# Optimization experiments

Hardware: AMD Instinct MI355X
Metric: run time of the kernel (lower is better)

## Reference

```python
import jax, jax.numpy as jnp
import numpy as np

N, E, G = 50000, 800000, 512
IN, HID, H1, H2, OUT = 128, 32, 8, 4, 128
D1, D2 = HID * H1, HID * H2  # 256, 128


def _ln(x, g, b, eps=1e-5):
    m = x.mean(-1, keepdims=True)
    v = jnp.var(x, axis=-1, keepdims=True)
    return (x - m) * jax.lax.rsqrt(v + eps) * g + b


def _gat_conv(x, W, a_src, a_dst, bias, edge_index, heads, ch, concat):
    # PyG GATConv (eval): h = xW per head; e = leakyrelu(a_src.h_src + a_dst.h_dst);
    # segment softmax over destination nodes; scatter-sum messages; self-loops added.
    n = x.shape[0]
    h = (x @ W).reshape(n, heads, ch)                      # [N,H,C]
    asrc = jnp.sum(h * a_src, axis=-1)                     # [N,H]
    adst = jnp.sum(h * a_dst, axis=-1)                     # [N,H]
    loop = jnp.arange(n)
    src = jnp.concatenate([edge_index[0], loop])           # [E+N]
    dst = jnp.concatenate([edge_index[1], loop])
    e = jax.nn.leaky_relu(asrc[src] + adst[dst], 0.2)      # [E+N,H]
    emax = jax.ops.segment_max(e, dst, num_segments=n)
    p = jnp.exp(e - emax[dst])
    denom = jax.ops.segment_sum(p, dst, num_segments=n)
    alpha = p / (denom[dst] + 1e-16)                       # [E+N,H]
    out = jax.ops.segment_sum(h[src] * alpha[..., None], dst, num_segments=n)  # [N,H,C]
    out = out.reshape(n, heads * ch) if concat else out.mean(axis=1)
    return out + bias


def setup_inputs():
    key = jax.random.key(0)
    ks = jax.random.split(key, 32)
    g = lambda i, shape, s=0.05: jax.random.normal(ks[i], shape, dtype=jnp.float32) * s
    inp = {
        "x": jax.random.normal(ks[0], (N, IN), dtype=jnp.float32),
        "edge_index": jax.random.randint(ks[1], (2, E), 0, N, dtype=jnp.int32),
        "batch": jnp.sort(jax.random.randint(ks[2], (N,), 0, G, dtype=jnp.int32)),
        # GAT layer 1: in 128 -> 8 heads x 32
        "W1": g(3, (IN, H1 * HID)), "a_src1": g(4, (H1, HID)), "a_dst1": g(5, (H1, HID)),
        "b1": jnp.zeros((D1,), jnp.float32), "g1": jnp.ones((D1,), jnp.float32), "be1": jnp.zeros((D1,), jnp.float32),
        "pw1": g(6, (IN, D1)), "pb1": jnp.zeros((D1,), jnp.float32),
        # GAT layer 2: 256 -> 4 heads x 32
        "W2": g(7, (D1, H2 * HID)), "a_src2": g(8, (H2, HID)), "a_dst2": g(9, (H2, HID)),
        "b2": jnp.zeros((D2,), jnp.float32), "g2": jnp.ones((D2,), jnp.float32), "be2": jnp.zeros((D2,), jnp.float32),
        "pw2": g(10, (D1, D2)), "pb2": jnp.zeros((D2,), jnp.float32),
        # GAT layer 3: 128 -> 1 head x 128, concat=False
        "W3": g(11, (D2, OUT)), "a_src3": g(12, (1, OUT)), "a_dst3": g(13, (1, OUT)),
        "b3": jnp.zeros((OUT,), jnp.float32), "g3": jnp.ones((OUT,), jnp.float32), "be3": jnp.zeros((OUT,), jnp.float32),
        "pw3": g(14, (D2, OUT)), "pb3": jnp.zeros((OUT,), jnp.float32),
    }
    return inp


def reference(x, edge_index, batch,
              W1, a_src1, a_dst1, b1, g1, be1, pw1, pb1,
              W2, a_src2, a_dst2, b2, g2, be2, pw2, pb2,
              W3, a_src3, a_dst3, b3, g3, be3, pw3, pb3):
    h1 = _gat_conv(x, W1, a_src1, a_dst1, b1, edge_index, H1, HID, True)
    h1 = jax.nn.elu(_ln(h1, g1, be1) + (x @ pw1 + pb1))
    h2 = _gat_conv(h1, W2, a_src2, a_dst2, b2, edge_index, H2, HID, True)
    h2 = jax.nn.elu(_ln(h2, g2, be2) + (h1 @ pw2 + pb2))
    h3 = _gat_conv(h2, W3, a_src3, a_dst3, b3, edge_index, 1, OUT, False)
    h3 = jax.nn.elu(_ln(h3, g3, be3) + (h2 @ pw3 + pb3))
    # jk='last' -> h3; global mean pool per graph
    sums = jax.ops.segment_sum(h3, batch, num_segments=G)              # [G,OUT]
    cnt = jax.ops.segment_sum(jnp.ones((N,), h3.dtype), batch, num_segments=G)
    return sums / jnp.maximum(cnt, 1.0)[:, None]
```

## Files before the change

### kernel.cpp

```cpp
#include <hip/hip_runtime.h>
#include <hip/hip_fp16.h>
#include <math.h>


typedef _Float16 f16x8 __attribute__((ext_vector_type(8)));
typedef float f32x4 __attribute__((ext_vector_type(4)));

static __device__ __forceinline__ float h2f(unsigned short u) {
  return __half2float(__builtin_bit_cast(__half, u));
}
static __device__ __forceinline__ unsigned short f2h(float f) {
  return __builtin_bit_cast(unsigned short, __float2half_rn(f));
}
static __device__ __forceinline__ float hlo(unsigned int w) {
  return __low2float(__builtin_bit_cast(__half2, w));
}
static __device__ __forceinline__ float hhi(unsigned int w) {
  return __high2float(__builtin_bit_cast(__half2, w));
}
static __device__ __forceinline__ float wave_sum(float v) {
#pragma unroll
  for (int off = 1; off < 64; off <<= 1) v += __shfl_xor(v, off, 64);
  return v;
}

template <int K, int C, int H, bool ATOMIC>
__global__ __launch_bounds__(256) void fused_gemm_kernel(
    const unsigned short* __restrict__ A, const unsigned short* __restrict__ Bp1,
    const unsigned short* __restrict__ Bp2, const float* __restrict__ bias2,
    const float* __restrict__ a_src, const float* __restrict__ a_dst,
    unsigned short* __restrict__ C1, unsigned short* __restrict__ C2,
    float* __restrict__ asrc, float* __restrict__ adst, int Ncols) {
  const int lane = threadIdx.x & 63;
  const int w = threadIdx.x >> 6;
  const int ml = lane & 15, kq = lane >> 4;
  const int row0 = blockIdx.y * 64 + (w >> 1) * 32;
  const int colt0 = blockIdx.x * 4 + (w & 1) * 2;
  constexpr int KB = K / 32;

  f32x4 w00 = {}, w01 = {}, w10 = {}, w11 = {};
  f32x4 p00 = {}, p01 = {}, p10 = {}, p11 = {};
  const unsigned short* a0 = A + (size_t)(row0 + ml) * K + kq * 8;
  const unsigned short* b1 = Bp1 + ((size_t)colt0 * KB * 64 + lane) * 8;
  const unsigned short* b2 = Bp2 + ((size_t)colt0 * KB * 64 + lane) * 8;
#pragma unroll
  for (int kb = 0; kb < KB; kb++) {
    f16x8 af0 = __builtin_bit_cast(f16x8, *(const uint4*)(a0 + kb * 32));
    f16x8 af1 = __builtin_bit_cast(f16x8, *(const uint4*)(a0 + 16 * K + kb * 32));
    f16x8 bw0 = __builtin_bit_cast(f16x8, *(const uint4*)(b1 + (size_t)kb * 512));
    f16x8 bw1 = __builtin_bit_cast(f16x8, *(const uint4*)(b1 + (size_t)(KB + kb) * 512));
    f16x8 bp0 = __builtin_bit_cast(f16x8, *(const uint4*)(b2 + (size_t)kb * 512));
    f16x8 bp1 = __builtin_bit_cast(f16x8, *(const uint4*)(b2 + (size_t)(KB + kb) * 512));
    w00 = __builtin_amdgcn_mfma_f32_16x16x32_f16(af0, bw0, w00, 0, 0, 0);
    w01 = __builtin_amdgcn_mfma_f32_16x16x32_f16(af0, bw1, w01, 0, 0, 0);
    w10 = __builtin_amdgcn_mfma_f32_16x16x32_f16(af1, bw0, w10, 0, 0, 0);
    w11 = __builtin_amdgcn_mfma_f32_16x16x32_f16(af1, bw1, w11, 0, 0, 0);
    p00 = __builtin_amdgcn_mfma_f32_16x16x32_f16(af0, bp0, p00, 0, 0, 0);
    p01 = __builtin_amdgcn_mfma_f32_16x16x32_f16(af0, bp1, p01, 0, 0, 0);
    p10 = __builtin_amdgcn_mfma_f32_16x16x32_f16(af1, bp0, p10, 0, 0, 0);
    p11 = __builtin_amdgcn_mfma_f32_16x16x32_f16(af1, bp1, p11, 0, 0, 0);
  }
  const int c0 = colt0 * 16 + ml, c1 = c0 + 16;
  const float bi0 = bias2[c0], bi1 = bias2[c1];
#pragma unroll
  for (int r = 0; r < 4; r++) {
    const size_t rA = (size_t)(row0 + kq * 4 + r);
    const size_t rB = rA + 16;
    C1[rA * Ncols + c0] = f2h(w00[r]);
    C1[rA * Ncols + c1] = f2h(w01[r]);
    C1[rB * Ncols + c0] = f2h(w10[r]);
    C1[rB * Ncols + c1] = f2h(w11[r]);
    C2[rA * Ncols + c0] = f2h(p00[r] + bi0);
    C2[rA * Ncols + c1] = f2h(p01[r] + bi1);
    C2[rB * Ncols + c0] = f2h(p10[r] + bi0);
    C2[rB * Ncols + c1] = f2h(p11[r] + bi1);
  }

  const int hh = (colt0 * 16) / C;
  const float aS0 = a_src[hh * C + (c0 % C)], aS1 = a_src[hh * C + (c1 % C)];
  const float aD0 = a_dst[hh * C + (c0 % C)], aD1 = a_dst[hh * C + (c1 % C)];
  float pS0[4], pD0[4], pS1[4], pD1[4];
#pragma unroll
  for (int r = 0; r < 4; r++) {
    pS0[r] = w00[r] * aS0 + w01[r] * aS1;
    pD0[r] = w00[r] * aD0 + w01[r] * aD1;
    pS1[r] = w10[r] * aS0 + w11[r] * aS1;
    pD1[r] = w10[r] * aD0 + w11[r] * aD1;
  }
#pragma unroll
  for (int off = 1; off < 16; off <<= 1) {
#pragma unroll
    for (int r = 0; r < 4; r++) {
      pS0[r] += __shfl_xor(pS0[r], off);
      pD0[r] += __shfl_xor(pD0[r], off);
      pS1[r] += __shfl_xor(pS1[r], off);
      pD1[r] += __shfl_xor(pD1[r], off);
    }
  }
  if (ml < 4) {
    const int r = ml;
    const int rowA = row0 + kq * 4 + r;
    const int rowB = rowA + 16;
    if constexpr (ATOMIC) {
      atomicAdd(&asrc[rowA * H + hh], pS0[r]);
      atomicAdd(&adst[rowA * H + hh], pD0[r]);
      atomicAdd(&asrc[rowB * H + hh], pS1[r]);
      atomicAdd(&adst[rowB * H + hh], pD1[r]);
    } else {
      asrc[rowA * H + hh] = pS0[r];
      adst[rowA * H + hh] = pD0[r];
      asrc[rowB * H + hh] = pS1[r];
      adst[rowB * H + hh] = pD1[r];
    }
  }
}

static __device__ __forceinline__ void repack_one(const float* B, unsigned short* Bp,
                                                  int K, int Ncols, int idx) {
  const int KB = K >> 5;
  const int lane = idx & 63;
  const int kb = (idx >> 6) % KB;
  const int nt = idx / (KB << 6);
  const int ml = lane & 15, kq = lane >> 4;
  unsigned short* dst = Bp + (size_t)idx * 8;
#pragma unroll
  for (int j = 0; j < 8; j++)
    dst[j] = f2h(B[(size_t)(kb * 32 + kq * 8 + j) * Ncols + nt * 16 + ml]);
}

__global__ __launch_bounds__(256) void repack_all_kernel(
    const float* W1, const float* pw1, const float* W2, const float* pw2,
    const float* W3, const float* pw3, unsigned short* BpW1, unsigned short* BpP1,
    unsigned short* BpW2, unsigned short* BpP2, unsigned short* BpW3,
    unsigned short* BpP3) {
  int idx = blockIdx.x * 256 + threadIdx.x;
  if (idx < 4096) { repack_one(W1, BpW1, 128, 256, idx); return; }
  idx -= 4096;
  if (idx < 4096) { repack_one(pw1, BpP1, 128, 256, idx); return; }
  idx -= 4096;
  if (idx < 4096) { repack_one(W2, BpW2, 256, 128, idx); return; }
  idx -= 4096;
  if (idx < 4096) { repack_one(pw2, BpP2, 256, 128, idx); return; }
  idx -= 4096;
  if (idx < 2048) { repack_one(W3, BpW3, 128, 128, idx); return; }
  idx -= 2048;
  repack_one(pw3, BpP3, 128, 128, idx);
}

__global__ void cast_f16_kernel(const float* __restrict__ src,
                                unsigned short* __restrict__ dst, int n4, int pad4) {
  const int i = blockIdx.x * 256 + threadIdx.x;
  if (i >= n4 + pad4) return;
  ushort4 o;
  if (i < n4) {
    float4 v = ((const float4*)src)[i];
    o.x = f2h(v.x); o.y = f2h(v.y); o.z = f2h(v.z); o.w = f2h(v.w);
  } else {
    o.x = o.y = o.z = o.w = 0;
  }
  ((ushort4*)dst)[i] = o;
}

__global__ void zero_pads_kernel(unsigned short* b256, unsigned short* b128, int pad) {
  const int i = blockIdx.x * 256 + threadIdx.x;
  if (i < pad * 256) b256[i] = 0;
  if (i < pad * 128) b128[i] = 0;
}

__global__ void zero2_kernel(float* a, float* b, int n) {
  const int i = blockIdx.x * 256 + threadIdx.x;
  if (i < n) { a[i] = 0.f; b[i] = 0.f; }
}

template <int H, int C, int SPLIT>
__global__ __launch_bounds__(256) void gat_agg_kernel(
    const unsigned short* __restrict__ hfeat, const float* __restrict__ asrc,
    const float* __restrict__ adst, const int* __restrict__ rowptr,
    const int* __restrict__ col, const float* __restrict__ bias,
    const float* __restrict__ gamma, const float* __restrict__ beta,
    const unsigned short* __restrict__ proj, unsigned short* __restrict__ out, int N) {
  constexpr int DOUT = H * C;
  constexpr int RL = DOUT / 16;
  static_assert(RL * SPLIT == 64, "bad split");
  constexpr int PD = 2;
  const int wave = threadIdx.x >> 6;
  const int lane = threadIdx.x & 63;
  const int n = blockIdx.x * 4 + wave;
  if (n >= N) return;
  const int rl = lane % RL;
  const int sub = lane / RL;
  const int c0 = rl * 16;
  const int myh = c0 / C;
  const int start = rowptr[n];
  const int deg = rowptr[n + 1] - start;
  const int vlen = deg + 1;
  const int nsteps = (vlen + SPLIT - 1) / SPLIT;
  const int ngroups = (nsteps + PD - 1) / PD;
  const float my_adl = adst[n * H + myh];
  const int clmax = (deg > 0) ? deg - 1 : 0;

  const __half2 hz = __float2half2_rn(0.f);
  __half2 acc2[8] = {hz, hz, hz, hz, hz, hz, hz, hz};
  float psum = 0.f;

  float aA[PD], aB[PD];
  uint4 h0A[PD], h1A[PD], h0B[PD], h1B[PD];

  auto issue = [&](int g, float* a, uint4* h0, uint4* h1) {
#pragma unroll
    for (int k = 0; k < PD; k++) {
      const int j = (g * PD + k) * SPLIT + sub;
      int s = col[start + min(j, clmax)];
      s = (j < deg) ? s : n;
      a[k] = asrc[s * H + myh];
      const unsigned short* hp = &hfeat[(size_t)s * DOUT + c0];
      h0[k] = *(const uint4*)hp;
      h1[k] = *(const uint4*)(hp + 8);
    }
  };
  auto consume = [&](int g, const float* a, const uint4* h0, const uint4* h1) {
#pragma unroll
    for (int k = 0; k < PD; k++) {
      const int j = (g * PD + k) * SPLIT + sub;
      float e = a[k] + my_adl;
      e = fmaxf(e, 0.2f * e);
      float p = __expf(e);
      p = (j < vlen) ? p : 0.f;
      psum += p;
      const __half2 pp = __float2half2_rn(p);
      acc2[0] = __hfma2(__builtin_bit_cast(__half2, h0[k].x), pp, acc2[0]);
      acc2[1] = __hfma2(__builtin_bit_cast(__half2, h0[k].y), pp, acc2[1]);
      acc2[2] = __hfma2(__builtin_bit_cast(__half2, h0[k].z), pp, acc2[2]);
      acc2[3] = __hfma2(__builtin_bit_cast(__half2, h0[k].w), pp, acc2[3]);
      acc2[4] = __hfma2(__builtin_bit_cast(__half2, h1[k].x), pp, acc2[4]);
      acc2[5] = __hfma2(__builtin_bit_cast(__half2, h1[k].y), pp, acc2[5]);
      acc2[6] = __hfma2(__builtin_bit_cast(__half2, h1[k].z), pp, acc2[6]);
      acc2[7] = __hfma2(__builtin_bit_cast(__half2, h1[k].w), pp, acc2[7]);
    }
  };

  issue(0, aA, h0A, h1A);
  for (int g = 0; g < ngroups; g += 2) {
    if (g + 1 < ngroups) issue(g + 1, aB, h0B, h1B);
    consume(g, aA, h0A, h1A);
    if (g + 1 < ngroups) {
      if (g + 2 < ngroups) issue(g + 2, aA, h0A, h1A);
      consume(g + 1, aB, h0B, h1B);
    }
  }

  float acc[16];
#pragma unroll
  for (int i = 0; i < 8; i++) {
    acc[2 * i] = __low2float(acc2[i]);
    acc[2 * i + 1] = __high2float(acc2[i]);
  }
#pragma unroll
  for (int o = RL; o < 64; o <<= 1) {
    psum += __shfl_xor(psum, o);
#pragma unroll
    for (int i = 0; i < 16; i++) acc[i] += __shfl_xor(acc[i], o);
  }

  const float rs = 1.f / (psum + 1e-16f);
  float v[16];
#pragma unroll
  for (int q = 0; q < 4; q++) {
    const float4 bi = *(const float4*)&bias[c0 + q * 4];
    v[q * 4 + 0] = acc[q * 4 + 0] * rs + bi.x;
    v[q * 4 + 1] = acc[q * 4 + 1] * rs + bi.y;
    v[q * 4 + 2] = acc[q * 4 + 2] * rs + bi.z;
    v[q * 4 + 3] = acc[q * 4 + 3] * rs + bi.w;
  }
  float s16 = 0.f;
#pragma unroll
  for (int i = 0; i < 16; i++) s16 += v[i];
  const float mean = wave_sum(s16) / (float)(DOUT * SPLIT);
  float q16 = 0.f;
#pragma unroll
  for (int i = 0; i < 16; i++) {
    v[i] -= mean;
    q16 += v[i] * v[i];
  }
  const float var = wave_sum(q16) / (float)(DOUT * SPLIT);
  const float rstd = rsqrtf(var + 1e-5f);

  const uint4 pr0 = *(const uint4*)&proj[(size_t)n * DOUT + c0];
  const uint4 pr1 = *(const uint4*)&proj[(size_t)n * DOUT + c0 + 8];
  float pres[16];
  pres[0] = hlo(pr0.x); pres[1] = hhi(pr0.x); pres[2] = hlo(pr0.y); pres[3] = hhi(pr0.y);
  pres[4] = hlo(pr0.z); pres[5] = hhi(pr0.z); pres[6] = hlo(pr0.w); pres[7] = hhi(pr0.w);
  pres[8] = hlo(pr1.x); pres[9] = hhi(pr1.x); pres[10] = hlo(pr1.y); pres[11] = hhi(pr1.y);
  pres[12] = hlo(pr1.z); pres[13] = hhi(pr1.z); pres[14] = hlo(pr1.w); pres[15] = hhi(pr1.w);

  float o16[16];
#pragma unroll
  for (int q = 0; q < 4; q++) {
    const float4 ga = *(const float4*)&gamma[c0 + q * 4];
    const float4 be = *(const float4*)&beta[c0 + q * 4];
    o16[q * 4 + 0] = v[q * 4 + 0] * rstd * ga.x + be.x + pres[q * 4 + 0];
    o16[q * 4 + 1] = v[q * 4 + 1] * rstd * ga.y + be.y + pres[q * 4 + 1];
    o16[q * 4 + 2] = v[q * 4 + 2] * rstd * ga.z + be.z + pres[q * 4 + 2];
    o16[q * 4 + 3] = v[q * 4 + 3] * rstd * ga.w + be.w + pres[q * 4 + 3];
  }
#pragma unroll
  for (int i = 0; i < 16; i++)
    o16[i] = (o16[i] > 0.f) ? o16[i] : (__expf(o16[i]) - 1.f);

  if (sub == 0) {
    uint4 ov0, ov1;
    ov0.x = (unsigned int)f2h(o16[0]) | ((unsigned int)f2h(o16[1]) << 16);
    ov0.y = (unsigned int)f2h(o16[2]) | ((unsigned int)f2h(o16[3]) << 16);
    ov0.z = (unsigned int)f2h(o16[4]) | ((unsigned int)f2h(o16[5]) << 16);
    ov0.w = (unsigned int)f2h(o16[6]) | ((unsigned int)f2h(o16[7]) << 16);
    ov1.x = (unsigned int)f2h(o16[8]) | ((unsigned int)f2h(o16[9]) << 16);
    ov1.y = (unsigned int)f2h(o16[10]) | ((unsigned int)f2h(o16[11]) << 16);
    ov1.z = (unsigned int)f2h(o16[12]) | ((unsigned int)f2h(o16[13]) << 16);
    ov1.w = (unsigned int)f2h(o16[14]) | ((unsigned int)f2h(o16[15]) << 16);
    *(uint4*)&out[(size_t)n * DOUT + c0] = ov0;
    *(uint4*)&out[(size_t)n * DOUT + c0 + 8] = ov1;
  }
}

__global__ void hist_kernel(const int* __restrict__ dst, int* __restrict__ cnt, int E) {
  const int e = blockIdx.x * 256 + threadIdx.x;
  if (e < E) atomicAdd(&cnt[dst[e]], 1);
}

__global__ __launch_bounds__(256) void scan1_kernel(int* __restrict__ cnt,
                                                    int* __restrict__ sums, int N) {
  __shared__ int sm[256];
  const int i = blockIdx.x * 256 + threadIdx.x;
  const int v = (i < N) ? cnt[i] : 0;
  sm[threadIdx.x] = v;
  __syncthreads();
  for (int off = 1; off < 256; off <<= 1) {
    const int t = (threadIdx.x >= off) ? sm[threadIdx.x - off] : 0;
    __syncthreads();
    sm[threadIdx.x] += t;
    __syncthreads();
  }
  if (i < N) cnt[i] = sm[threadIdx.x] - v;
  if (threadIdx.x == 255) sums[blockIdx.x] = sm[255];
}

__global__ __launch_bounds__(256) void scan2_kernel(int* __restrict__ sums, int nb) {
  __shared__ int sm[256];
  const int v = (threadIdx.x < nb) ? sums[threadIdx.x] : 0;
  sm[threadIdx.x] = v;
  __syncthreads();
  for (int off = 1; off < 256; off <<= 1) {
    const int t = (threadIdx.x >= off) ? sm[threadIdx.x - off] : 0;
    __syncthreads();
    sm[threadIdx.x] += t;
    __syncthreads();
  }
  if (threadIdx.x < nb) sums[threadIdx.x] = sm[threadIdx.x] - v;
}

__global__ void scan3_kernel(const int* __restrict__ cnt, const int* __restrict__ sums,
                             int* __restrict__ rowptr, int* __restrict__ cursor,
                             int N, int E) {
  const int i = blockIdx.x * 256 + threadIdx.x;
  if (i < N) {
    const int r = cnt[i] + sums[blockIdx.x];
    rowptr[i] = r;
    cursor[i] = r;
  }
  if (i == 0) rowptr[N] = E;
}

__global__ void scatter_kernel(const int* __restrict__ src, const int* __restrict__ dst,
                               int* __restrict__ cursor, int* __restrict__ col, int E) {
  const int e = blockIdx.x * 256 + threadIdx.x;
  if (e < E) {
    const int p = atomicAdd(&cursor[dst[e]], 1);
    col[p] = src[e];
  }
}

__global__ __launch_bounds__(128) void pool_kernel(const unsigned short* __restrict__ h3,
                                                   const int* __restrict__ batch,
                                                   float* __restrict__ out, int N) {
  __shared__ int sse[2];
  const int g = blockIdx.x;
  if (threadIdx.x == 0) {
    int lo = 0, hi = N;
    while (lo < hi) { const int mid = (lo + hi) >> 1; if (batch[mid] < g) lo = mid + 1; else hi = mid; }
    sse[0] = lo;
    lo = 0; hi = N;
    while (lo < hi) { const int mid = (lo + hi) >> 1; if (batch[mid] < g + 1) lo = mid + 1; else hi = mid; }
    sse[1] = lo;
  }
  __syncthreads();
  const int s = sse[0], e = sse[1];
  float sum = 0.f;
  for (int r = s; r < e; r++) sum += h2f(h3[(size_t)r * 128 + threadIdx.x]);
  out[g * 128 + threadIdx.x] = (e > s) ? sum / (float)(e - s) : 0.f;
}

extern "C" void kernel_launch(void* const* d_in, const int* in_sizes, int n_in,
                              void* d_out, int out_size, void* d_ws, size_t ws_size,
                              hipStream_t stream) {
  const float* x      = (const float*)d_in[0];
  const int* edge_idx = (const int*)d_in[1];
  const int* batch    = (const int*)d_in[2];
  const float* W1     = (const float*)d_in[3];
  const float* a_src1 = (const float*)d_in[4];
  const float* a_dst1 = (const float*)d_in[5];
  const float* b1     = (const float*)d_in[6];
  const float* g1     = (const float*)d_in[7];
  const float* be1    = (const float*)d_in[8];
  const float* pw1    = (const float*)d_in[9];
  const float* pb1    = (const float*)d_in[10];
  const float* W2     = (const float*)d_in[11];
  const float* a_src2 = (const float*)d_in[12];
  const float* a_dst2 = (const float*)d_in[13];
  const float* b2     = (const float*)d_in[14];
  const float* g2     = (const float*)d_in[15];
  const float* be2    = (const float*)d_in[16];
  const float* pw2    = (const float*)d_in[17];
  const float* pb2    = (const float*)d_in[18];
  const float* W3     = (const float*)d_in[19];
  const float* a_src3 = (const float*)d_in[20];
  const float* a_dst3 = (const float*)d_in[21];
  const float* b3     = (const float*)d_in[22];
  const float* g3     = (const float*)d_in[23];
  const float* be3    = (const float*)d_in[24];
  const float* pw3    = (const float*)d_in[25];
  const float* pb3    = (const float*)d_in[26];

  const int NN = in_sizes[0] / 128;
  const int E  = in_sizes[1] / 2;
  const int G  = out_size / 128;
  const int M64 = (NN + 63) & ~63;

  size_t off = 0;
  auto alloc = [&](size_t bytes) {
    size_t r = off;
    off += (bytes + 255) & ~(size_t)255;
    return r;
  };
  char* ws = (char*)d_ws;
  unsigned short* big0 = (unsigned short*)(ws + alloc((size_t)M64 * 256 * 2));
  unsigned short* big1 = (unsigned short*)(ws + alloc((size_t)M64 * 256 * 2));
  unsigned short* s0   = (unsigned short*)(ws + alloc((size_t)M64 * 128 * 2));
  unsigned short* s1   = (unsigned short*)(ws + alloc((size_t)M64 * 128 * 2));
  unsigned short* projb = (unsigned short*)(ws + alloc((size_t)M64 * 256 * 2));
  float* asrcB = (float*)(ws + alloc((size_t)M64 * 8 * 4));
  float* adstB = (float*)(ws + alloc((size_t)M64 * 8 * 4));
  int* rowptr  = (int*)(ws + alloc((size_t)(NN + 1) * 4));
  int* cnt     = (int*)(ws + alloc((size_t)NN * 4));
  int* cursor  = (int*)(ws + alloc((size_t)NN * 4));
  int* colb    = (int*)(ws + alloc((size_t)(E + 64) * 4));
  int* sums    = (int*)(ws + alloc(256 * 4));
  unsigned short* BpW1 = (unsigned short*)(ws + alloc(128 * 256 * 2));
  unsigned short* BpP1 = (unsigned short*)(ws + alloc(128 * 256 * 2));
  unsigned short* BpW2 = (unsigned short*)(ws + alloc(256 * 128 * 2));
  unsigned short* BpP2 = (unsigned short*)(ws + alloc(256 * 128 * 2));
  unsigned short* BpW3 = (unsigned short*)(ws + alloc(128 * 128 * 2));
  unsigned short* BpP3 = (unsigned short*)(ws + alloc(128 * 128 * 2));
  (void)ws_size; (void)n_in;

  const int EB = (E + 255) / 256;
  const int NB = (NN + 255) / 256;
  const int NW = (NN + 3) / 4;
  const int MB = M64 / 64;
  const int pad = M64 - NN;

  hipMemsetAsync(cnt, 0, (size_t)NN * 4, stream);
  hist_kernel<<<EB, 256, 0, stream>>>(edge_idx + E, cnt, E);
  scan1_kernel<<<NB, 256, 0, stream>>>(cnt, sums, NN);
  scan2_kernel<<<1, 256, 0, stream>>>(sums, NB);
  scan3_kernel<<<NB, 256, 0, stream>>>(cnt, sums, rowptr, cursor, NN, E);
  scatter_kernel<<<EB, 256, 0, stream>>>(edge_idx, edge_idx + E, cursor, colb, E);

  cast_f16_kernel<<<(M64 * 128 / 4 + 255) / 256, 256, 0, stream>>>(x, s0, NN * 32, pad * 32);
  if (pad)
    zero_pads_kernel<<<(pad * 256 + 255) / 256, 256, 0, stream>>>(
        big1 + (size_t)NN * 256, s1 + (size_t)NN * 128, pad);

  repack_all_kernel<<<80, 256, 0, stream>>>(W1, pw1, W2, pw2, W3, pw3,
                                            BpW1, BpP1, BpW2, BpP2, BpW3, BpP3);

  fused_gemm_kernel<128, 32, 8, false><<<dim3(4, MB), 256, 0, stream>>>(
      s0, BpW1, BpP1, pb1, a_src1, a_dst1, big0, projb, asrcB, adstB, 256);
  gat_agg_kernel<8, 32, 4><<<NW, 256, 0, stream>>>(big0, asrcB, adstB, rowptr, colb,
                                                   b1, g1, be1, projb, big1, NN);

  fused_gemm_kernel<256, 32, 4, false><<<dim3(2, MB), 256, 0, stream>>>(
      big1, BpW2, BpP2, pb2, a_src2, a_dst2, s0, projb, asrcB, adstB, 128);
  gat_agg_kernel<4, 32, 8><<<NW, 256, 0, stream>>>(s0, asrcB, adstB, rowptr, colb,
                                                   b2, g2, be2, projb, s1, NN);

  zero2_kernel<<<(M64 + 255) / 256, 256, 0, stream>>>(asrcB, adstB, M64);
  fused_gemm_kernel<128, 128, 1, true><<<dim3(2, MB), 256, 0, stream>>>(
      s1, BpW3, BpP3, pb3, a_src3, a_dst3, big0, projb, asrcB, adstB, 128);
  gat_agg_kernel<1, 128, 8><<<NW, 256, 0, stream>>>(big0, asrcB, adstB, rowptr, colb,
                                                    b3, g3, be3, projb, s0, NN);

  pool_kernel<<<G, 128, 0, stream>>>(s0, batch, (float*)d_out, NN);
}
```

Baseline: 508.9 us.

## Stage GEMM outputs through LDS and merge small setup kernels into one

The fused GEMM epilogue now writes its f16 tiles into shared memory and then stores them to global memory as coalesced 16-byte rows, replacing scattered 2-byte stores. The cast, memset, pad zeroing, layer-3 score zeroing and weight repack are folded into a single init kernel. scan2 and scan3 are merged into one kernel, and layer 3 gets its own score buffers so that zeroing can happen up front. This cuts launch count and uncoalesced store traffic, at the cost of extra LDS use and a block barrier in the GEMM.

```diff
diff --git a/kernel.cpp b/kernel.cpp
--- a/kernel.cpp
+++ b/kernel.cpp
@@ -31,6 +31,8 @@
     const float* __restrict__ a_src, const float* __restrict__ a_dst,
     unsigned short* __restrict__ C1, unsigned short* __restrict__ C2,
     float* __restrict__ asrc, float* __restrict__ adst, int Ncols) {
+  __shared__ unsigned short t1[64 * 72];
+  __shared__ unsigned short t2[64 * 72];
   const int lane = threadIdx.x & 63;
   const int w = threadIdx.x >> 6;
   const int ml = lane & 15, kq = lane >> 4;
@@ -62,18 +64,19 @@
   }
   const int c0 = colt0 * 16 + ml, c1 = c0 + 16;
   const float bi0 = bias2[c0], bi1 = bias2[c1];
+
+  const int lr0 = (w >> 1) * 32 + kq * 4;
+  const int lc0 = (w & 1) * 32 + ml;
 #pragma unroll
   for (int r = 0; r < 4; r++) {
-    const size_t rA = (size_t)(row0 + kq * 4 + r);
-    const size_t rB = rA + 16;
-    C1[rA * Ncols + c0] = f2h(w00[r]);
-    C1[rA * Ncols + c1] = f2h(w01[r]);
-    C1[rB * Ncols + c0] = f2h(w10[r]);
-    C1[rB * Ncols + c1] = f2h(w11[r]);
-    C2[rA * Ncols + c0] = f2h(p00[r] + bi0);
-    C2[rA * Ncols + c1] = f2h(p01[r] + bi1);
-    C2[rB * Ncols + c0] = f2h(p10[r] + bi0);
-    C2[rB * Ncols + c1] = f2h(p11[r] + bi1);
+    t1[(lr0 + r) * 72 + lc0] = f2h(w00[r]);
+    t1[(lr0 + r) * 72 + lc0 + 16] = f2h(w01[r]);
+    t1[(lr0 + 16 + r) * 72 + lc0] = f2h(w10[r]);
+    t1[(lr0 + 16 + r) * 72 + lc0 + 16] = f2h(w11[r]);
+    t2[(lr0 + r) * 72 + lc0] = f2h(p00[r] + bi0);
+    t2[(lr0 + r) * 72 + lc0 + 16] = f2h(p01[r] + bi1);
+    t2[(lr0 + 16 + r) * 72 + lc0] = f2h(p10[r] + bi0);
+    t2[(lr0 + 16 + r) * 72 + lc0 + 16] = f2h(p11[r] + bi1);
   }
 
   const int hh = (colt0 * 16) / C;
@@ -113,6 +116,18 @@
       adst[rowB * H + hh] = pD1[r];
     }
   }
+
+  __syncthreads();
+  const int lr = threadIdx.x >> 3;
+  const int ch = (threadIdx.x & 7) * 8;
+  const int gcol = blockIdx.x * 64 + ch;
+#pragma unroll
+  for (int pass = 0; pass < 2; pass++) {
+    const int row = lr + pass * 32;
+    const size_t g = (size_t)(blockIdx.y * 64 + row) * Ncols + gcol;
+    *(uint4*)&C1[g] = *(const uint4*)&t1[row * 72 + ch];
+    *(uint4*)&C2[g] = *(const uint4*)&t2[row * 72 + ch];
+  }
 }
 
 static __device__ __forceinline__ void repack_one(const float* B, unsigned short* Bp,
@@ -128,12 +143,39 @@
     dst[j] = f2h(B[(size_t)(kb * 32 + kq * 8 + j) * Ncols + nt * 16 + ml]);
 }
 
-__global__ __launch_bounds__(256) void repack_all_kernel(
-    const float* W1, const float* pw1, const float* W2, const float* pw2,
-    const float* W3, const float* pw3, unsigned short* BpW1, unsigned short* BpP1,
-    unsigned short* BpW2, unsigned short* BpP2, unsigned short* BpW3,
-    unsigned short* BpP3) {
+__global__ __launch_bounds__(256) void init_kernel(
+    const float* __restrict__ x, unsigned short* __restrict__ xh, int n4, int NN,
+    int M64, int pad, int* __restrict__ cnt, unsigned short* __restrict__ big1pad,
+    unsigned short* __restrict__ s1pad, float* __restrict__ asrc3,
+    float* __restrict__ adst3, const float* W1, const float* pw1, const float* W2,
+    const float* pw2, const float* W3, const float* pw3, unsigned short* BpW1,
+    unsigned short* BpP1, unsigned short* BpW2, unsigned short* BpP2,
+    unsigned short* BpW3, unsigned short* BpP3) {
   int idx = blockIdx.x * 256 + threadIdx.x;
+  const int castN = M64 * 32;
+  if (idx < castN) {
+    ushort4 o;
+    if (idx < n4) {
+      float4 v = ((const float4*)x)[idx];
+      o.x = f2h(v.x); o.y = f2h(v.y); o.z = f2h(v.z); o.w = f2h(v.w);
+    } else {
+      o.x = o.y = o.z = o.w = 0;
+    }
+    ((ushort4*)xh)[idx] = o;
+    return;
+  }
+  idx -= castN;
+  if (idx < NN) { cnt[idx] = 0; return; }
+  idx -= NN;
+  if (idx < pad * 32) { ((uint4*)big1pad)[idx] = uint4{0, 0, 0, 0}; return; }
+  idx -= pad * 32;
+  if (idx < pad * 16) { ((uint4*)s1pad)[idx] = uint4{0, 0, 0, 0}; return; }
+  idx -= pad * 16;
+  const int zf = M64 / 4;
+  if (idx < zf) { ((float4*)asrc3)[idx] = float4{0.f, 0.f, 0.f, 0.f}; return; }
+  idx -= zf;
+  if (idx < zf) { ((float4*)adst3)[idx] = float4{0.f, 0.f, 0.f, 0.f}; return; }
+  idx -= zf;
   if (idx < 4096) { repack_one(W1, BpW1, 128, 256, idx); return; }
   idx -= 4096;
   if (idx < 4096) { repack_one(pw1, BpP1, 128, 256, idx); return; }
@@ -144,32 +186,7 @@
   idx -= 4096;
   if (idx < 2048) { repack_one(W3, BpW3, 128, 128, idx); return; }
   idx -= 2048;
-  repack_one(pw3, BpP3, 128, 128, idx);
-}
-
-__global__ void cast_f16_kernel(const float* __restrict__ src,
-                                unsigned short* __restrict__ dst, int n4, int pad4) {
-  const int i = blockIdx.x * 256 + threadIdx.x;
-  if (i >= n4 + pad4) return;
-  ushort4 o;
-  if (i < n4) {
-    float4 v = ((const float4*)src)[i];
-    o.x = f2h(v.x); o.y = f2h(v.y); o.z = f2h(v.z); o.w = f2h(v.w);
-  } else {
-    o.x = o.y = o.z = o.w = 0;
-  }
-  ((ushort4*)dst)[i] = o;
-}
-
-__global__ void zero_pads_kernel(unsigned short* b256, unsigned short* b128, int pad) {
-  const int i = blockIdx.x * 256 + threadIdx.x;
-  if (i < pad * 256) b256[i] = 0;
-  if (i < pad * 128) b128[i] = 0;
-}
-
-__global__ void zero2_kernel(float* a, float* b, int n) {
-  const int i = blockIdx.x * 256 + threadIdx.x;
-  if (i < n) { a[i] = 0.f; b[i] = 0.f; }
+  if (idx < 2048) repack_one(pw3, BpP3, 128, 128, idx);
 }
 
 template <int H, int C, int SPLIT>
@@ -344,7 +361,11 @@
   if (threadIdx.x == 255) sums[blockIdx.x] = sm[255];
 }
 
-__global__ __launch_bounds__(256) void scan2_kernel(int* __restrict__ sums, int nb) {
+__global__ __launch_bounds__(256) void scan23_kernel(const int* __restrict__ cnt,
+                                                     const int* __restrict__ sums,
+                                                     int* __restrict__ rowptr,
+                                                     int* __restrict__ cursor, int N,
+                                                     int E, int nb) {
   __shared__ int sm[256];
   const int v = (threadIdx.x < nb) ? sums[threadIdx.x] : 0;
   sm[threadIdx.x] = v;
@@ -355,15 +376,10 @@
     sm[threadIdx.x] += t;
     __syncthreads();
   }
-  if (threadIdx.x < nb) sums[threadIdx.x] = sm[threadIdx.x] - v;
-}
-
-__global__ void scan3_kernel(const int* __restrict__ cnt, const int* __restrict__ sums,
-                             int* __restrict__ rowptr, int* __restrict__ cursor,
-                             int N, int E) {
+  const int base = (blockIdx.x == 0) ? 0 : sm[blockIdx.x - 1];
   const int i = blockIdx.x * 256 + threadIdx.x;
   if (i < N) {
-    const int r = cnt[i] + sums[blockIdx.x];
+    const int r = cnt[i] + base;
     rowptr[i] = r;
     cursor[i] = r;
   }
@@ -447,8 +463,10 @@
   unsigned short* s0   = (unsigned short*)(ws + alloc((size_t)M64 * 128 * 2));
   unsigned short* s1   = (unsigned short*)(ws + alloc((size_t)M64 * 128 * 2));
   unsigned short* projb = (unsigned short*)(ws + alloc((size_t)M64 * 256 * 2));
-  float* asrcB = (float*)(ws + alloc((size_t)M64 * 8 * 4));
-  float* adstB = (float*)(ws + alloc((size_t)M64 * 8 * 4));
+  float* asrcB  = (float*)(ws + alloc((size_t)M64 * 8 * 4));
+  float* adstB  = (float*)(ws + alloc((size_t)M64 * 8 * 4));
+  float* asrc3B = (float*)(ws + alloc((size_t)M64 * 4));
+  float* adst3B = (float*)(ws + alloc((size_t)M64 * 4));
   int* rowptr  = (int*)(ws + alloc((size_t)(NN + 1) * 4));
   int* cnt     = (int*)(ws + alloc((size_t)NN * 4));
   int* cursor  = (int*)(ws + alloc((size_t)NN * 4));
@@ -468,20 +486,16 @@
   const int MB = M64 / 64;
   const int pad = M64 - NN;
 
-  hipMemsetAsync(cnt, 0, (size_t)NN * 4, stream);
+  const int initN = M64 * 32 + NN + pad * 32 + pad * 16 + 2 * (M64 / 4) + 20480;
+  init_kernel<<<(initN + 255) / 256, 256, 0, stream>>>(
+      x, s0, NN * 32, NN, M64, pad, cnt, big1 + (size_t)NN * 256,
+      s1 + (size_t)NN * 128, asrc3B, adst3B, W1, pw1, W2, pw2, W3, pw3, BpW1, BpP1,
+      BpW2, BpP2, BpW3, BpP3);
+
   hist_kernel<<<EB, 256, 0, stream>>>(edge_idx + E, cnt, E);
   scan1_kernel<<<NB, 256, 0, stream>>>(cnt, sums, NN);
-  scan2_kernel<<<1, 256, 0, stream>>>(sums, NB);
-  scan3_kernel<<<NB, 256, 0, stream>>>(cnt, sums, rowptr, cursor, NN, E);
+  scan23_kernel<<<NB, 256, 0, stream>>>(cnt, sums, rowptr, cursor, NN, E, NB);
   scatter_kernel<<<EB, 256, 0, stream>>>(edge_idx, edge_idx + E, cursor, colb, E);
-
-  cast_f16_kernel<<<(M64 * 128 / 4 + 255) / 256, 256, 0, stream>>>(x, s0, NN * 32, pad * 32);
-  if (pad)
-    zero_pads_kernel<<<(pad * 256 + 255) / 256, 256, 0, stream>>>(
-        big1 + (size_t)NN * 256, s1 + (size_t)NN * 128, pad);
-
-  repack_all_kernel<<<80, 256, 0, stream>>>(W1, pw1, W2, pw2, W3, pw3,
-                                            BpW1, BpP1, BpW2, BpP2, BpW3, BpP3);
 
   fused_gemm_kernel<128, 32, 8, false><<<dim3(4, MB), 256, 0, stream>>>(
       s0, BpW1, BpP1, pb1, a_src1, a_dst1, big0, projb, asrcB, adstB, 256);
@@ -493,10 +507,9 @@
   gat_agg_kernel<4, 32, 8><<<NW, 256, 0, stream>>>(s0, asrcB, adstB, rowptr, colb,
                                                    b2, g2, be2, projb, s1, NN);
 
-  zero2_kernel<<<(M64 + 255) / 256, 256, 0, stream>>>(asrcB, adstB, M64);
   fused_gemm_kernel<128, 128, 1, true><<<dim3(2, MB), 256, 0, stream>>>(
-      s1, BpW3, BpP3, pb3, a_src3, a_dst3, big0, projb, asrcB, adstB, 128);
-  gat_agg_kernel<1, 128, 8><<<NW, 256, 0, stream>>>(big0, asrcB, adstB, rowptr, colb,
+      s1, BpW3, BpP3, pb3, a_src3, a_dst3, big0, projb, asrc3B, adst3B, 128);
+  gat_agg_kernel<1, 128, 8><<<NW, 256, 0, stream>>>(big0, asrc3B, adst3B, rowptr, colb,
                                                     b3, g3, be3, projb, s0, NN);
 
   pool_kernel<<<G, 128, 0, stream>>>(s0, batch, (float*)d_out, NN);
```

Result: faster. 484.9 us (-4.7%).
